# Kernel optimization log

Hardware: AMD Instinct MI355X
Metric: run time of the kernel (lower is better)

The kernel has to match this reference:

```python
import jax, jax.numpy as jnp
import numpy as np

B, S, Y = 2, 4, 4          # samples, n_views (B*S = BS), voxel height vox_xyz_size[1]
BS = B * S

def _bilinear(feat, coords):
    # feat: [C,H,W]; coords: [N,2] normalized (x,y); OOB handled by the valid mask
    C, H, W = feat.shape
    gx, gy = coords[:, 0], coords[:, 1]
    ix = (gx + 1.0) * 0.5 * (W - 1)
    iy = (gy + 1.0) * 0.5 * (H - 1)
    x0 = jnp.floor(ix); y0 = jnp.floor(iy)
    wx = ix - x0; wy = iy - y0
    x0i = jnp.clip(x0.astype(jnp.int32), 0, W - 1); x1i = jnp.clip(x0i + 1, 0, W - 1)
    y0i = jnp.clip(y0.astype(jnp.int32), 0, H - 1); y1i = jnp.clip(y0i + 1, 0, H - 1)
    v00 = feat[:, y0i, x0i]; v01 = feat[:, y0i, x1i]
    v10 = feat[:, y1i, x0i]; v11 = feat[:, y1i, x1i]
    out = (v00 * (1 - wx) * (1 - wy) + v01 * wx * (1 - wy)
           + v10 * (1 - wx) * wy + v11 * wx * wy)            # [C,N]
    valid = (gx >= -1) & (gx <= 1) & (gy >= -1) & (gy <= 1)   # [N]
    return out, valid

def _scale(feat, coords, Zs, Xs, w, b):
    # feat: [BS,C,H,W]; coords: [BS, Y*Zs*Xs, 2]; w: [Co, C*Y]; b: [Co]
    C = feat.shape[1]
    samp, valid = jax.vmap(_bilinear)(feat, coords)           # [BS,C,N], [BS,N]
    samp = samp.reshape(BS, C, Y, Zs * Xs)
    masked = samp * valid.reshape(BS, 1, Y, Zs * Xs).astype(samp.dtype)
    v = masked.reshape(B, S, C * Y, Zs * Xs).max(axis=1)      # max-pool across views
    v = v.reshape(B, C * Y, Zs, Xs)                           # BEV grid
    bev = jax.nn.silu(jnp.einsum('bizx,oi->bozx', v, w) + b[None, :, None, None])
    return bev, valid

def setup_inputs():
    key = jax.random.key(0)
    ks = jax.random.split(key, 9)
    f = jnp.float32
    x3 = jax.random.normal(ks[0], (BS, 256, 64, 64), f)
    x4 = jax.random.normal(ks[1], (BS, 512, 32, 32), f)
    x5 = jax.random.normal(ks[2], (BS, 1024, 16, 16), f)
    coords_s2 = jax.random.uniform(ks[3], (BS, Y * 64 * 64, 2), f) * 2.4 - 1.2
    coords_s4 = jax.random.uniform(ks[4], (BS, Y * 32 * 32, 2), f) * 2.4 - 1.2
    coords_s8 = jax.random.uniform(ks[5], (BS, Y * 16 * 16, 2), f) * 2.4 - 1.2
    w2 = jax.random.normal(ks[6], (256, 256 * Y), f) * 0.02
    b2 = jnp.zeros((256,), f)
    w4 = jax.random.normal(ks[7], (512, 512 * Y), f) * 0.02
    b4 = jnp.zeros((512,), f)
    w8 = jax.random.normal(ks[8], (1024, 1024 * Y), f) * 0.02
    b8 = jnp.zeros((1024,), f)
    return {"x3": x3, "x4": x4, "x5": x5,
            "coords_s2": coords_s2, "coords_s4": coords_s4, "coords_s8": coords_s8,
            "w2": w2, "b2": b2, "w4": w4, "b4": b4, "w8": w8, "b8": b8}

def reference(x3, x4, x5, coords_s2, coords_s4, coords_s8, w2, b2, w4, b4, w8, b8):
    bev2, valid2 = _scale(x3, coords_s2, 64, 64, w2, b2)
    bev4, _ = _scale(x4, coords_s4, 32, 32, w4, b4)
    bev8, _ = _scale(x5, coords_s8, 16, 16, w8, b8)
    valid_vox_mask = valid2.reshape(B, S, -1).max(axis=1).astype(jnp.float32)
    return bev2, bev4, bev8, valid_vox_mask
```

## Files before the change

### kernel.cpp

```cpp
#include <hip/hip_runtime.h>
#include <hip/hip_bf16.h>
#include <math.h>

namespace {

constexpr int B_ = 2;
constexpr int S_ = 4;

typedef short short8 __attribute__((ext_vector_type(8)));
typedef float floatx4 __attribute__((ext_vector_type(4)));
typedef unsigned short ushort4v __attribute__((ext_vector_type(4)));
typedef unsigned short ushort8v __attribute__((ext_vector_type(8)));

__device__ __forceinline__ unsigned short f2bf(float x) {
    union { float f; unsigned u; } a; a.f = x;
    unsigned r = a.u + 0x7fff + ((a.u >> 16) & 1);
    return (unsigned short)(r >> 16);
}
__device__ __forceinline__ float bf2f(unsigned short h) {
    union { unsigned u; float f; } a; a.u = ((unsigned)h) << 16;
    return a.f;
}

__device__ __forceinline__ void transp_tile(
    const float* __restrict__ in, unsigned short* __restrict__ out,
    int C, int P, int bs, int pBase, int cBase, int tid, float (*tile)[33])
{
    int tx = tid & 31;
    int ty = tid >> 5;
    const float* ip = in + ((size_t)bs * C + cBase) * P + pBase;
    #pragma unroll
    for (int r = 0; r < 32; r += 8)
        tile[ty + r][tx] = ip[(size_t)(ty + r) * P + tx];
    __syncthreads();
    unsigned short* op = out + ((size_t)bs * P + pBase) * C + cBase;
    #pragma unroll
    for (int r = 0; r < 32; r += 8)
        op[(size_t)(ty + r) * C + tx] = f2bf(tile[tx][ty + r]);
}

__global__ __launch_bounds__(256) void transpose_all(
    const float* __restrict__ x3, const float* __restrict__ x4, const float* __restrict__ x5,
    unsigned short* __restrict__ f2, unsigned short* __restrict__ f4, unsigned short* __restrict__ f8)
{
    __shared__ float tile[32][33];
    int bid = blockIdx.x;
    int tid = threadIdx.x;
    if (bid < 8192) {
        int local = bid;
        int bs = local >> 10, r = local & 1023;
        transp_tile(x3, f2, 256, 4096, bs, (r & 127) * 32, (r >> 7) * 32, tid, tile);
    } else if (bid < 12288) {
        int local = bid - 8192;
        int bs = local >> 9, r = local & 511;
        transp_tile(x4, f4, 512, 1024, bs, (r & 31) * 32, (r >> 5) * 32, tid, tile);
    } else {
        int local = bid - 12288;
        int bs = local >> 8, r = local & 255;
        transp_tile(x5, f8, 1024, 256, bs, (r & 7) * 32, (r >> 3) * 32, tid, tile);
    }
}

__global__ __launch_bounds__(256) void cvt_w_all(
    const float* __restrict__ w2, const float* __restrict__ w4, const float* __restrict__ w8,
    unsigned short* __restrict__ o2, unsigned short* __restrict__ o4, unsigned short* __restrict__ o8)
{
    int bid = blockIdx.x;
    const float* in; unsigned short* out; int local;
    if (bid < 256)       { in = w2; out = o2; local = bid; }
    else if (bid < 1280) { in = w4; out = o4; local = bid - 256; }
    else                 { in = w8; out = o8; local = bid - 1280; }
    long idx = ((long)local * 256 + threadIdx.x) * 4;
    float4 v = *reinterpret_cast<const float4*>(in + idx);
    ushort4 u;
    u.x = f2bf(v.x); u.y = f2bf(v.y); u.z = f2bf(v.z); u.w = f2bf(v.w);
    *reinterpret_cast<ushort4*>(out + idx) = u;
}

__device__ __forceinline__ void sample_wave(
    const unsigned short* __restrict__ featT, const float* __restrict__ coords,
    unsigned short* __restrict__ vout,
    int Wd, int M, int C, int logM, int logCc, int wid, int lane)
{
    int chunk = wid & ((1 << logCc) - 1);
    int m = (wid >> logCc) & (M - 1);
    int b = wid >> (logCc + logM);
    int c = chunk * 256 + lane * 4;
    int P = Wd * Wd;

    unsigned short outv[16];
    #pragma unroll
    for (int y = 0; y < 4; ++y) {
        float bst0 = -3.4e38f, bst1 = -3.4e38f, bst2 = -3.4e38f, bst3 = -3.4e38f;
        bool anyinv = false;
        #pragma unroll
        for (int s = 0; s < 4; ++s) {
            int bs = b * S_ + s;
            float2 g = ((const float2*)coords)[((size_t)bs << (logM + 2)) + ((size_t)y << logM) + m];
            bool valid = (g.x >= -1.f) && (g.x <= 1.f) && (g.y >= -1.f) && (g.y <= 1.f);
            if (!valid) { anyinv = true; continue; }
            float ix = (g.x + 1.f) * 0.5f * (float)(Wd - 1);
            float iy = (g.y + 1.f) * 0.5f * (float)(Wd - 1);
            float x0f = floorf(ix), y0f = floorf(iy);
            float wx = ix - x0f, wy = iy - y0f;
            int x0 = min(max((int)x0f, 0), Wd - 1);
            int x1 = min(x0 + 1, Wd - 1);
            int y0 = min(max((int)y0f, 0), Wd - 1);
            int y1 = min(y0 + 1, Wd - 1);
            float w00 = (1.f - wx) * (1.f - wy);
            float w01 = wx * (1.f - wy);
            float w10 = (1.f - wx) * wy;
            float w11 = wx * wy;
            const unsigned short* fp = featT + (size_t)bs * P * C + c;
            ushort4v u00 = *reinterpret_cast<const ushort4v*>(fp + (size_t)(y0 * Wd + x0) * C);
            ushort4v u01 = *reinterpret_cast<const ushort4v*>(fp + (size_t)(y0 * Wd + x1) * C);
            ushort4v u10 = *reinterpret_cast<const ushort4v*>(fp + (size_t)(y1 * Wd + x0) * C);
            ushort4v u11 = *reinterpret_cast<const ushort4v*>(fp + (size_t)(y1 * Wd + x1) * C);
            bst0 = fmaxf(bst0, bf2f(u00[0]) * w00 + bf2f(u01[0]) * w01 + bf2f(u10[0]) * w10 + bf2f(u11[0]) * w11);
            bst1 = fmaxf(bst1, bf2f(u00[1]) * w00 + bf2f(u01[1]) * w01 + bf2f(u10[1]) * w10 + bf2f(u11[1]) * w11);
            bst2 = fmaxf(bst2, bf2f(u00[2]) * w00 + bf2f(u01[2]) * w01 + bf2f(u10[2]) * w10 + bf2f(u11[2]) * w11);
            bst3 = fmaxf(bst3, bf2f(u00[3]) * w00 + bf2f(u01[3]) * w01 + bf2f(u10[3]) * w10 + bf2f(u11[3]) * w11);
        }
        if (anyinv) {
            bst0 = fmaxf(bst0, 0.f); bst1 = fmaxf(bst1, 0.f);
            bst2 = fmaxf(bst2, 0.f); bst3 = fmaxf(bst3, 0.f);
        }
        outv[0 * 4 + y] = f2bf(bst0);
        outv[1 * 4 + y] = f2bf(bst1);
        outv[2 * 4 + y] = f2bf(bst2);
        outv[3 * 4 + y] = f2bf(bst3);
    }
    size_t base = (((size_t)b << logM) + m) * ((size_t)C * 4) + chunk * 1024 + lane * 16;
    ushort8v o0, o1;
    #pragma unroll
    for (int t = 0; t < 8; ++t) { o0[t] = outv[t]; o1[t] = outv[8 + t]; }
    *reinterpret_cast<ushort8v*>(vout + base)     = o0;
    *reinterpret_cast<ushort8v*>(vout + base + 8) = o1;
}

__global__ __launch_bounds__(256) void sample_all(
    const unsigned short* __restrict__ f2, const unsigned short* __restrict__ f4,
    const unsigned short* __restrict__ f8,
    const float* __restrict__ c2, const float* __restrict__ c4, const float* __restrict__ c8,
    unsigned short* __restrict__ v2, unsigned short* __restrict__ v4,
    unsigned short* __restrict__ v8)
{
    int gw = (int)((blockIdx.x * 256 + threadIdx.x) >> 6);
    int lane = threadIdx.x & 63;
    if (gw < 8192)
        sample_wave(f2, c2, v2, 64, 4096, 256, 12, 0, gw, lane);
    else if (gw < 12288)
        sample_wave(f4, c4, v4, 32, 1024, 512, 10, 1, gw - 8192, lane);
    else
        sample_wave(f8, c8, v8, 16, 256, 1024, 8, 2, gw - 12288, lane);
}

#define GLOAD(s, it) do { \
    w##s##a = *reinterpret_cast<const float4*>(Wp + (size_t)row0 * K + (it) * 64 + kc); \
    w##s##b = *reinterpret_cast<const float4*>(Wp + (size_t)(row0 + 32) * K + (it) * 64 + kc); \
    v##s##a = *reinterpret_cast<const float4*>(Vp + (size_t)row0 * K + (it) * 64 + kc); \
    v##s##b = *reinterpret_cast<const float4*>(Vp + (size_t)(row0 + 32) * K + (it) * 64 + kc); \
} while (0)

#define LSTORE(s, buf) do { \
    *reinterpret_cast<float4*>(&As[buf][row0 * 72 + kc]) = w##s##a; \
    *reinterpret_cast<float4*>(&As[buf][(row0 + 32) * 72 + kc]) = w##s##b; \
    *reinterpret_cast<float4*>(&Bs[buf][row0 * 72 + kc]) = v##s##a; \
    *reinterpret_cast<float4*>(&Bs[buf][(row0 + 32) * 72 + kc]) = v##s##b; \
} while (0)

#define MFMA_STEP(buf) do { \
    _Pragma("unroll") \
    for (int kss = 0; kss < 64; kss += 32) { \
        short8 af0 = *reinterpret_cast<const short8*>(&As[buf][(wo + lr) * 72 + kss + quad * 8]); \
        short8 af1 = *reinterpret_cast<const short8*>(&As[buf][(wo + 16 + lr) * 72 + kss + quad * 8]); \
        short8 bf0 = *reinterpret_cast<const short8*>(&Bs[buf][(wm + lr) * 72 + kss + quad * 8]); \
        short8 bf1 = *reinterpret_cast<const short8*>(&Bs[buf][(wm + 16 + lr) * 72 + kss + quad * 8]); \
        acc[0][0] = __builtin_amdgcn_mfma_f32_16x16x32_bf16(af0, bf0, acc[0][0], 0, 0, 0); \
        acc[0][1] = __builtin_amdgcn_mfma_f32_16x16x32_bf16(af0, bf1, acc[0][1], 0, 0, 0); \
        acc[1][0] = __builtin_amdgcn_mfma_f32_16x16x32_bf16(af1, bf0, acc[1][0], 0, 0, 0); \
        acc[1][1] = __builtin_amdgcn_mfma_f32_16x16x32_bf16(af1, bf1, acc[1][1], 0, 0, 0); \
    } \
} while (0)

__device__ __forceinline__ void gemm_tile(
    const unsigned short* __restrict__ Wb, const unsigned short* __restrict__ Vb,
    const float* __restrict__ bias, float* __restrict__ out, float* __restrict__ partial,
    int N, int K, int M, int kSplit, int local, int logMt, int logNt,
    int tid, unsigned short (*As)[64 * 72], unsigned short (*Bs)[64 * 72])
{
    const int mTile = local & ((1 << logMt) - 1);
    const int rest  = local >> logMt;
    const int oTile = rest & ((1 << logNt) - 1);
    const int z     = rest >> logNt;
    const int b = z & 1;
    const int ks = z >> 1;
    const int Kspan = K / kSplit;
    const int nIter = Kspan >> 6;

    const int mBase = mTile * 64;
    const int oBase = oTile * 64;
    const int lane = tid & 63;
    const int wave = tid >> 6;
    const int wo = (wave >> 1) * 32;
    const int wm = (wave & 1) * 32;
    const int quad = lane >> 4;
    const int lr = lane & 15;
    const int row0 = tid >> 3;
    const int kc = (tid & 7) * 8;

    const unsigned short* Wp = Wb + (size_t)oBase * K + ks * Kspan;
    const unsigned short* Vp = Vb + ((size_t)b * M + mBase) * K + ks * Kspan;

    floatx4 acc[2][2] = {};
    float4 w0a, w0b, v0a, v0b;
    float4 w1a, w1b, v1a, v1b;

    GLOAD(0, 0);
    LSTORE(0, 0);
    GLOAD(1, 1);
    __syncthreads();

    for (int it = 0; it < nIter; it += 2) {
        MFMA_STEP(0);
        LSTORE(1, 1);
        if (it + 2 < nIter) GLOAD(0, it + 2);
        __syncthreads();
        MFMA_STEP(1);
        if (it + 2 < nIter) {
            LSTORE(0, 0);
            if (it + 3 < nIter) GLOAD(1, it + 3);
            __syncthreads();
        }
    }

    if (kSplit == 1) {
        #pragma unroll
        for (int i = 0; i < 2; ++i)
            #pragma unroll
            for (int r = 0; r < 4; ++r) {
                int o = oBase + wo + i * 16 + quad * 4 + r;
                float bi = bias[o];
                #pragma unroll
                for (int j = 0; j < 2; ++j) {
                    int m = mBase + wm + j * 16 + lr;
                    float x = acc[i][j][r] + bi;
                    out[((size_t)b * N + o) * M + m] = x / (1.f + __expf(-x));
                }
            }
    } else {
        float* pp = partial + (size_t)z * N * M;
        #pragma unroll
        for (int i = 0; i < 2; ++i)
            #pragma unroll
            for (int r = 0; r < 4; ++r) {
                int o = oBase + wo + i * 16 + quad * 4 + r;
                #pragma unroll
                for (int j = 0; j < 2; ++j) {
                    int m = mBase + wm + j * 16 + lr;
                    pp[(size_t)o * M + m] = acc[i][j][r];
                }
            }
    }
}

__global__ __launch_bounds__(256) void gemm_all(
    const unsigned short* __restrict__ w2b, const unsigned short* __restrict__ w4b,
    const unsigned short* __restrict__ w8b,
    const unsigned short* __restrict__ v2, const unsigned short* __restrict__ v4,
    const unsigned short* __restrict__ v8,
    const float* __restrict__ b2, float* __restrict__ bev2,
    float* __restrict__ part4, float* __restrict__ part8)
{
    __shared__ __align__(16) unsigned short As[2][64 * 72];
    __shared__ __align__(16) unsigned short Bs[2][64 * 72];
    int bid = blockIdx.x;
    int tid = threadIdx.x;
    if (bid < 512)
        gemm_tile(w2b, v2, b2, bev2, nullptr, 256, 1024, 4096, 1, bid, 6, 2, tid, As, Bs);
    else if (bid < 1536)
        gemm_tile(w4b, v4, nullptr, nullptr, part4, 512, 2048, 1024, 4, bid - 512, 4, 3, tid, As, Bs);
    else
        gemm_tile(w8b, v8, nullptr, nullptr, part8, 1024, 4096, 256, 8, bid - 1536, 2, 4, tid, As, Bs);
}

__device__ __forceinline__ void reduce_seg(
    const float* __restrict__ partial, const float* __restrict__ bias,
    float* __restrict__ out, int N, int M, int kSplit, size_t idx)
{
    int m4 = M >> 2;
    int mi = (int)(idx % m4);
    int o  = (int)((idx / m4) % N);
    int b  = (int)(idx / ((size_t)m4 * N));
    size_t base = ((size_t)b * N + o) * M + (size_t)mi * 4;
    size_t stride = (size_t)2 * N * M;
    float4 s = *reinterpret_cast<const float4*>(partial + base);
    for (int k = 1; k < kSplit; ++k) {
        float4 t = *reinterpret_cast<const float4*>(partial + base + (size_t)k * stride);
        s.x += t.x; s.y += t.y; s.z += t.z; s.w += t.w;
    }
    float bi = bias[o];
    float xs[4] = {s.x + bi, s.y + bi, s.z + bi, s.w + bi};
    float4 r;
    r.x = xs[0] / (1.f + __expf(-xs[0]));
    r.y = xs[1] / (1.f + __expf(-xs[1]));
    r.z = xs[2] / (1.f + __expf(-xs[2]));
    r.w = xs[3] / (1.f + __expf(-xs[3]));
    *reinterpret_cast<float4*>(out + base) = r;
}

__global__ __launch_bounds__(256) void reduce_mask_all(
    const float* __restrict__ part4, const float* __restrict__ b4, float* __restrict__ bev4,
    const float* __restrict__ part8, const float* __restrict__ b8, float* __restrict__ bev8,
    const float* __restrict__ c2, float* __restrict__ mask)
{
    int bid = blockIdx.x;
    int tid = threadIdx.x;
    if (bid < 1024) {
        reduce_seg(part4, b4, bev4, 512, 1024, 4, (size_t)bid * 256 + tid);
    } else if (bid < 1536) {
        reduce_seg(part8, b8, bev8, 1024, 256, 8, (size_t)(bid - 1024) * 256 + tid);
    } else {
        int idx = (bid - 1536) * 256 + tid;
        int n = idx & 16383;
        int b = idx >> 14;
        float best = 0.f;
        #pragma unroll
        for (int s = 0; s < S_; ++s) {
            float2 g = ((const float2*)c2)[(size_t)(b * S_ + s) * 16384 + n];
            bool valid = (g.x >= -1.f) && (g.x <= 1.f) && (g.y >= -1.f) && (g.y <= 1.f);
            if (valid) best = 1.f;
        }
        mask[idx] = best;
    }
}

}

extern "C" void kernel_launch(void* const* d_in, const int* in_sizes, int n_in,
                              void* d_out, int out_size, void* d_ws, size_t ws_size,
                              hipStream_t stream)
{
    const float* x3 = (const float*)d_in[0];
    const float* x4 = (const float*)d_in[1];
    const float* x5 = (const float*)d_in[2];
    const float* c2 = (const float*)d_in[3];
    const float* c4 = (const float*)d_in[4];
    const float* c8 = (const float*)d_in[5];
    const float* w2 = (const float*)d_in[6];
    const float* b2 = (const float*)d_in[7];
    const float* w4 = (const float*)d_in[8];
    const float* b4 = (const float*)d_in[9];
    const float* w8 = (const float*)d_in[10];
    const float* b8 = (const float*)d_in[11];

    float* out  = (float*)d_out;
    float* bev2 = out;
    float* bev4 = bev2 + (long)2 * 256 * 64 * 64;
    float* bev8 = bev4 + (long)2 * 512 * 32 * 32;
    float* mask = bev8 + (long)2 * 1024 * 16 * 16;

    char* ws = (char*)d_ws;
    unsigned short* f2v  = (unsigned short*)(ws);
    unsigned short* f4v  = (unsigned short*)(ws + (16L << 20));
    unsigned short* f8v  = (unsigned short*)(ws + (24L << 20));
    unsigned short* v2v  = (unsigned short*)(ws + (28L << 20));
    unsigned short* v4v  = (unsigned short*)(ws + (44L << 20));
    unsigned short* v8v  = (unsigned short*)(ws + (52L << 20));
    unsigned short* w2bf = (unsigned short*)(ws + (56L << 20));
    unsigned short* w4bf = (unsigned short*)(ws + (57L << 20));
    unsigned short* w8bf = (unsigned short*)(ws + (59L << 20));
    float*          part4 = (float*)(ws + (68L << 20));
    float*          part8 = (float*)(ws + (84L << 20));

    transpose_all<<<dim3(14336), 256, 0, stream>>>(x3, x4, x5, f2v, f4v, f8v);
    cvt_w_all<<<dim3(5376), 256, 0, stream>>>(w2, w4, w8, w2bf, w4bf, w8bf);
    sample_all<<<dim3(3584), 256, 0, stream>>>(f2v, f4v, f8v, c2, c4, c8, v2v, v4v, v8v);
    gemm_all<<<dim3(2560), 256, 0, stream>>>(w2bf, w4bf, w8bf, v2v, v4v, v8v,
                                             b2, bev2, part4, part8);
    reduce_mask_all<<<dim3(1664), 256, 0, stream>>>(part4, b4, bev4, part8, b8, bev8,
                                                    c2, mask);
}
```

Baseline: 210.0 us.

## Precompute bilinear coordinate table, merge prep kernels, and widen sampling to 8 channels

Transposes, weight conversion, a new coordinate-prep pass and the validity mask are merged into one launch. The prep pass stores packed bilinear corner indices and fp16 weights per sample. The sampling kernel reads this table instead of recomputing coordinates for every channel chunk, and each lane loads 8 bf16 channels per corner instead of 4, halving the wave count. This removes one kernel launch and redundant coordinate math, at the cost of an extra table in the workspace and fp16-rounded interpolation weights.

```diff
diff --git a/kernel.cpp b/kernel.cpp
--- a/kernel.cpp
+++ b/kernel.cpp
@@ -4,12 +4,8 @@
 
 namespace {
 
-constexpr int B_ = 2;
-constexpr int S_ = 4;
-
 typedef short short8 __attribute__((ext_vector_type(8)));
 typedef float floatx4 __attribute__((ext_vector_type(4)));
-typedef unsigned short ushort4v __attribute__((ext_vector_type(4)));
 typedef unsigned short ushort8v __attribute__((ext_vector_type(8)));
 
 __device__ __forceinline__ unsigned short f2bf(float x) {
@@ -20,6 +16,16 @@
 __device__ __forceinline__ float bf2f(unsigned short h) {
     union { unsigned u; float f; } a; a.u = ((unsigned)h) << 16;
     return a.f;
+}
+__device__ __forceinline__ unsigned f2h(float x) {
+    _Float16 h = (_Float16)x;
+    unsigned short u; __builtin_memcpy(&u, &h, 2);
+    return u;
+}
+__device__ __forceinline__ float h2f(unsigned u) {
+    unsigned short us = (unsigned short)u;
+    _Float16 h; __builtin_memcpy(&h, &us, 2);
+    return (float)h;
 }
 
 __device__ __forceinline__ void transp_tile(
@@ -39,120 +45,162 @@
         op[(size_t)(ty + r) * C + tx] = f2bf(tile[tx][ty + r]);
 }
 
-__global__ __launch_bounds__(256) void transpose_all(
+__device__ __forceinline__ void coord_prep(
+    const float* __restrict__ coords, uint4* __restrict__ table, int Wd, int idx)
+{
+    float2 g = ((const float2*)coords)[idx];
+    uint4 e;
+    bool valid = (g.x >= -1.f) && (g.x <= 1.f) && (g.y >= -1.f) && (g.y <= 1.f);
+    if (!valid) {
+        e.x = 0xFFFFFFFFu; e.y = 0u; e.z = 0u; e.w = 0u;
+    } else {
+        float ix = (g.x + 1.f) * 0.5f * (float)(Wd - 1);
+        float iy = (g.y + 1.f) * 0.5f * (float)(Wd - 1);
+        float x0f = floorf(ix), y0f = floorf(iy);
+        float wx = ix - x0f, wy = iy - y0f;
+        int x0 = min(max((int)x0f, 0), Wd - 1);
+        int x1 = min(x0 + 1, Wd - 1);
+        int y0 = min(max((int)y0f, 0), Wd - 1);
+        int y1 = min(y0 + 1, Wd - 1);
+        unsigned p00 = y0 * Wd + x0, p01 = y0 * Wd + x1;
+        unsigned p10 = y1 * Wd + x0, p11 = y1 * Wd + x1;
+        e.x = p00 | (p01 << 16);
+        e.y = p10 | (p11 << 16);
+        e.z = f2h((1.f - wx) * (1.f - wy)) | (f2h(wx * (1.f - wy)) << 16);
+        e.w = f2h((1.f - wx) * wy)         | (f2h(wx * wy) << 16);
+    }
+    table[idx] = e;
+}
+
+__global__ __launch_bounds__(256) void prep_all(
     const float* __restrict__ x3, const float* __restrict__ x4, const float* __restrict__ x5,
-    unsigned short* __restrict__ f2, unsigned short* __restrict__ f4, unsigned short* __restrict__ f8)
+    unsigned short* __restrict__ f2, unsigned short* __restrict__ f4, unsigned short* __restrict__ f8,
+    const float* __restrict__ w2, const float* __restrict__ w4, const float* __restrict__ w8,
+    unsigned short* __restrict__ o2, unsigned short* __restrict__ o4, unsigned short* __restrict__ o8,
+    const float* __restrict__ c2, const float* __restrict__ c4, const float* __restrict__ c8,
+    uint4* __restrict__ t2, uint4* __restrict__ t4, uint4* __restrict__ t8,
+    float* __restrict__ mask)
 {
     __shared__ float tile[32][33];
     int bid = blockIdx.x;
     int tid = threadIdx.x;
     if (bid < 8192) {
-        int local = bid;
-        int bs = local >> 10, r = local & 1023;
+        int bs = bid >> 10, r = bid & 1023;
         transp_tile(x3, f2, 256, 4096, bs, (r & 127) * 32, (r >> 7) * 32, tid, tile);
     } else if (bid < 12288) {
         int local = bid - 8192;
         int bs = local >> 9, r = local & 511;
         transp_tile(x4, f4, 512, 1024, bs, (r & 31) * 32, (r >> 5) * 32, tid, tile);
-    } else {
+    } else if (bid < 14336) {
         int local = bid - 12288;
         int bs = local >> 8, r = local & 255;
         transp_tile(x5, f8, 1024, 256, bs, (r & 7) * 32, (r >> 3) * 32, tid, tile);
-    }
-}
-
-__global__ __launch_bounds__(256) void cvt_w_all(
-    const float* __restrict__ w2, const float* __restrict__ w4, const float* __restrict__ w8,
-    unsigned short* __restrict__ o2, unsigned short* __restrict__ o4, unsigned short* __restrict__ o8)
-{
-    int bid = blockIdx.x;
-    const float* in; unsigned short* out; int local;
-    if (bid < 256)       { in = w2; out = o2; local = bid; }
-    else if (bid < 1280) { in = w4; out = o4; local = bid - 256; }
-    else                 { in = w8; out = o8; local = bid - 1280; }
-    long idx = ((long)local * 256 + threadIdx.x) * 4;
-    float4 v = *reinterpret_cast<const float4*>(in + idx);
-    ushort4 u;
-    u.x = f2bf(v.x); u.y = f2bf(v.y); u.z = f2bf(v.z); u.w = f2bf(v.w);
-    *reinterpret_cast<ushort4*>(out + idx) = u;
-}
-
-__device__ __forceinline__ void sample_wave(
-    const unsigned short* __restrict__ featT, const float* __restrict__ coords,
+    } else if (bid < 19712) {
+        int local = bid - 14336;
+        const float* in; unsigned short* out;
+        if (local < 256)       { in = w2; out = o2; }
+        else if (local < 1280) { in = w4; out = o4; local -= 256; }
+        else                   { in = w8; out = o8; local -= 1280; }
+        long idx = ((long)local * 256 + tid) * 4;
+        float4 v = *reinterpret_cast<const float4*>(in + idx);
+        ushort4 u;
+        u.x = f2bf(v.x); u.y = f2bf(v.y); u.z = f2bf(v.z); u.w = f2bf(v.w);
+        *reinterpret_cast<ushort4*>(out + idx) = u;
+    } else if (bid < 20224) {
+        coord_prep(c2, t2, 64, (bid - 19712) * 256 + tid);
+    } else if (bid < 20352) {
+        coord_prep(c4, t4, 32, (bid - 20224) * 256 + tid);
+    } else if (bid < 20384) {
+        coord_prep(c8, t8, 16, (bid - 20352) * 256 + tid);
+    } else {
+        int idx = (bid - 20384) * 256 + tid;
+        int n = idx & 16383;
+        int b = idx >> 14;
+        float best = 0.f;
+        #pragma unroll
+        for (int s = 0; s < 4; ++s) {
+            float2 g = ((const float2*)c2)[(size_t)(b * 4 + s) * 16384 + n];
+            bool valid = (g.x >= -1.f) && (g.x <= 1.f) && (g.y >= -1.f) && (g.y <= 1.f);
+            if (valid) best = 1.f;
+        }
+        mask[idx] = best;
+    }
+}
+
+__device__ __forceinline__ void sample_wave_v4(
+    const unsigned short* __restrict__ featT, const uint4* __restrict__ table,
     unsigned short* __restrict__ vout,
-    int Wd, int M, int C, int logM, int logCc, int wid, int lane)
-{
-    int chunk = wid & ((1 << logCc) - 1);
-    int m = (wid >> logCc) & (M - 1);
-    int b = wid >> (logCc + logM);
-    int c = chunk * 256 + lane * 4;
-    int P = Wd * Wd;
-
-    unsigned short outv[16];
+    int P, int M, int C, int logM, int mwLog, int ckLog, int wid, int lane)
+{
+    int cover = 64 >> mwLog;
+    int dm = (mwLog ? (lane >> (6 - mwLog)) : 0);
+    int laneInM = lane & (cover - 1);
+    int chunk = wid & ((1 << ckLog) - 1);
+    int rest = wid >> ckLog;
+    int mg = rest & ((M >> mwLog) - 1);
+    int b = rest >> (logM - mwLog);
+    int m = (mg << mwLog) + dm;
+    int ch = chunk * (cover * 8) + laneInM * 8;
+
+    unsigned short outv[32];
     #pragma unroll
     for (int y = 0; y < 4; ++y) {
-        float bst0 = -3.4e38f, bst1 = -3.4e38f, bst2 = -3.4e38f, bst3 = -3.4e38f;
+        float bst[8];
+        #pragma unroll
+        for (int j = 0; j < 8; ++j) bst[j] = -3.4e38f;
         bool anyinv = false;
         #pragma unroll
         for (int s = 0; s < 4; ++s) {
-            int bs = b * S_ + s;
-            float2 g = ((const float2*)coords)[((size_t)bs << (logM + 2)) + ((size_t)y << logM) + m];
-            bool valid = (g.x >= -1.f) && (g.x <= 1.f) && (g.y >= -1.f) && (g.y <= 1.f);
-            if (!valid) { anyinv = true; continue; }
-            float ix = (g.x + 1.f) * 0.5f * (float)(Wd - 1);
-            float iy = (g.y + 1.f) * 0.5f * (float)(Wd - 1);
-            float x0f = floorf(ix), y0f = floorf(iy);
-            float wx = ix - x0f, wy = iy - y0f;
-            int x0 = min(max((int)x0f, 0), Wd - 1);
-            int x1 = min(x0 + 1, Wd - 1);
-            int y0 = min(max((int)y0f, 0), Wd - 1);
-            int y1 = min(y0 + 1, Wd - 1);
-            float w00 = (1.f - wx) * (1.f - wy);
-            float w01 = wx * (1.f - wy);
-            float w10 = (1.f - wx) * wy;
-            float w11 = wx * wy;
-            const unsigned short* fp = featT + (size_t)bs * P * C + c;
-            ushort4v u00 = *reinterpret_cast<const ushort4v*>(fp + (size_t)(y0 * Wd + x0) * C);
-            ushort4v u01 = *reinterpret_cast<const ushort4v*>(fp + (size_t)(y0 * Wd + x1) * C);
-            ushort4v u10 = *reinterpret_cast<const ushort4v*>(fp + (size_t)(y1 * Wd + x0) * C);
-            ushort4v u11 = *reinterpret_cast<const ushort4v*>(fp + (size_t)(y1 * Wd + x1) * C);
-            bst0 = fmaxf(bst0, bf2f(u00[0]) * w00 + bf2f(u01[0]) * w01 + bf2f(u10[0]) * w10 + bf2f(u11[0]) * w11);
-            bst1 = fmaxf(bst1, bf2f(u00[1]) * w00 + bf2f(u01[1]) * w01 + bf2f(u10[1]) * w10 + bf2f(u11[1]) * w11);
-            bst2 = fmaxf(bst2, bf2f(u00[2]) * w00 + bf2f(u01[2]) * w01 + bf2f(u10[2]) * w10 + bf2f(u11[2]) * w11);
-            bst3 = fmaxf(bst3, bf2f(u00[3]) * w00 + bf2f(u01[3]) * w01 + bf2f(u10[3]) * w10 + bf2f(u11[3]) * w11);
+            int bs = b * 4 + s;
+            uint4 e = table[(((size_t)bs * 4 + y) << logM) + m];
+            if ((e.x & 0xffffu) == 0xffffu) { anyinv = true; continue; }
+            unsigned p00 = e.x & 0xffffu, p01 = e.x >> 16;
+            unsigned p10 = e.y & 0xffffu, p11 = e.y >> 16;
+            float w00 = h2f(e.z & 0xffffu), w01 = h2f(e.z >> 16);
+            float w10 = h2f(e.w & 0xffffu), w11 = h2f(e.w >> 16);
+            const unsigned short* fp = featT + (size_t)bs * P * C + ch;
+            ushort8v u00 = *reinterpret_cast<const ushort8v*>(fp + (size_t)p00 * C);
+            ushort8v u01 = *reinterpret_cast<const ushort8v*>(fp + (size_t)p01 * C);
+            ushort8v u10 = *reinterpret_cast<const ushort8v*>(fp + (size_t)p10 * C);
+            ushort8v u11 = *reinterpret_cast<const ushort8v*>(fp + (size_t)p11 * C);
+            #pragma unroll
+            for (int j = 0; j < 8; ++j) {
+                float v = bf2f(u00[j]) * w00 + bf2f(u01[j]) * w01
+                        + bf2f(u10[j]) * w10 + bf2f(u11[j]) * w11;
+                bst[j] = fmaxf(bst[j], v);
+            }
         }
-        if (anyinv) {
-            bst0 = fmaxf(bst0, 0.f); bst1 = fmaxf(bst1, 0.f);
-            bst2 = fmaxf(bst2, 0.f); bst3 = fmaxf(bst3, 0.f);
+        #pragma unroll
+        for (int j = 0; j < 8; ++j) {
+            float v = anyinv ? fmaxf(bst[j], 0.f) : bst[j];
+            outv[j * 4 + y] = f2bf(v);
         }
-        outv[0 * 4 + y] = f2bf(bst0);
-        outv[1 * 4 + y] = f2bf(bst1);
-        outv[2 * 4 + y] = f2bf(bst2);
-        outv[3 * 4 + y] = f2bf(bst3);
-    }
-    size_t base = (((size_t)b << logM) + m) * ((size_t)C * 4) + chunk * 1024 + lane * 16;
-    ushort8v o0, o1;
+    }
+    size_t base = (((size_t)b << logM) + m) * ((size_t)C * 4) + (size_t)ch * 4;
     #pragma unroll
-    for (int t = 0; t < 8; ++t) { o0[t] = outv[t]; o1[t] = outv[8 + t]; }
-    *reinterpret_cast<ushort8v*>(vout + base)     = o0;
-    *reinterpret_cast<ushort8v*>(vout + base + 8) = o1;
+    for (int t = 0; t < 4; ++t) {
+        ushort8v o;
+        #pragma unroll
+        for (int q = 0; q < 8; ++q) o[q] = outv[t * 8 + q];
+        *reinterpret_cast<ushort8v*>(vout + base + t * 8) = o;
+    }
 }
 
 __global__ __launch_bounds__(256) void sample_all(
     const unsigned short* __restrict__ f2, const unsigned short* __restrict__ f4,
     const unsigned short* __restrict__ f8,
-    const float* __restrict__ c2, const float* __restrict__ c4, const float* __restrict__ c8,
+    const uint4* __restrict__ t2, const uint4* __restrict__ t4, const uint4* __restrict__ t8,
     unsigned short* __restrict__ v2, unsigned short* __restrict__ v4,
     unsigned short* __restrict__ v8)
 {
     int gw = (int)((blockIdx.x * 256 + threadIdx.x) >> 6);
     int lane = threadIdx.x & 63;
-    if (gw < 8192)
-        sample_wave(f2, c2, v2, 64, 4096, 256, 12, 0, gw, lane);
-    else if (gw < 12288)
-        sample_wave(f4, c4, v4, 32, 1024, 512, 10, 1, gw - 8192, lane);
+    if (gw < 4096)
+        sample_wave_v4(f2, t2, v2, 4096, 4096, 256, 12, 1, 0, gw, lane);
+    else if (gw < 6144)
+        sample_wave_v4(f4, t4, v4, 1024, 1024, 512, 10, 0, 0, gw - 4096, lane);
     else
-        sample_wave(f8, c8, v8, 16, 256, 1024, 8, 2, gw - 12288, lane);
+        sample_wave_v4(f8, t8, v8, 256, 256, 1024, 8, 0, 1, gw - 6144, lane);
 }
 
 #define GLOAD(s, it) do { \
@@ -309,30 +357,16 @@
     *reinterpret_cast<float4*>(out + base) = r;
 }
 
-__global__ __launch_bounds__(256) void reduce_mask_all(
+__global__ __launch_bounds__(256) void reduce_all(
     const float* __restrict__ part4, const float* __restrict__ b4, float* __restrict__ bev4,
-    const float* __restrict__ part8, const float* __restrict__ b8, float* __restrict__ bev8,
-    const float* __restrict__ c2, float* __restrict__ mask)
+    const float* __restrict__ part8, const float* __restrict__ b8, float* __restrict__ bev8)
 {
     int bid = blockIdx.x;
     int tid = threadIdx.x;
-    if (bid < 1024) {
+    if (bid < 1024)
         reduce_seg(part4, b4, bev4, 512, 1024, 4, (size_t)bid * 256 + tid);
-    } else if (bid < 1536) {
+    else
         reduce_seg(part8, b8, bev8, 1024, 256, 8, (size_t)(bid - 1024) * 256 + tid);
-    } else {
-        int idx = (bid - 1536) * 256 + tid;
-        int n = idx & 16383;
-        int b = idx >> 14;
-        float best = 0.f;
-        #pragma unroll
-        for (int s = 0; s < S_; ++s) {
-            float2 g = ((const float2*)c2)[(size_t)(b * S_ + s) * 16384 + n];
-            bool valid = (g.x >= -1.f) && (g.x <= 1.f) && (g.y >= -1.f) && (g.y <= 1.f);
-            if (valid) best = 1.f;
-        }
-        mask[idx] = best;
-    }
 }
 
 }
@@ -372,12 +406,18 @@
     unsigned short* w8bf = (unsigned short*)(ws + (59L << 20));
     float*          part4 = (float*)(ws + (68L << 20));
     float*          part8 = (float*)(ws + (84L << 20));
-
-    transpose_all<<<dim3(14336), 256, 0, stream>>>(x3, x4, x5, f2v, f4v, f8v);
-    cvt_w_all<<<dim3(5376), 256, 0, stream>>>(w2, w4, w8, w2bf, w4bf, w8bf);
-    sample_all<<<dim3(3584), 256, 0, stream>>>(f2v, f4v, f8v, c2, c4, c8, v2v, v4v, v8v);
-    gemm_all<<<dim3(2560), 256, 0, stream>>>(w2bf, w4bf, w8bf, v2v, v4v, v8v,
-                                             b2, bev2, part4, part8);
-    reduce_mask_all<<<dim3(1664), 256, 0, stream>>>(part4, b4, bev4, part8, b8, bev8,
-                                                    c2, mask);
-}
+    uint4*          t2v   = (uint4*)(ws + (100L << 20));
+    uint4*          t4v   = (uint4*)(ws + (102L << 20));
+    uint4*          t8v   = (uint4*)(ws + (102L << 20) + (1L << 19));
+
+    prep_all<<<dim3(20512), 256, 0, stream>>>(
+        x3, x4, x5, f2v, f4v, f8v,
+        w2, w4, w8, w2bf, w4bf, w8bf,
+        c2, c4, c8, t2v, t4v, t8v, mask);
+    sample_all<<<dim3(1792), 256, 0, stream>>>(
+        f2v, f4v, f8v, t2v, t4v, t8v, v2v, v4v, v8v);
+    gemm_all<<<dim3(2560), 256, 0, stream>>>(
+        w2bf, w4bf, w8bf, v2v, v4v, v8v, b2, bev2, part4, part8);
+    reduce_all<<<dim3(1536), 256, 0, stream>>>(
+        part4, b4, bev4, part8, b8, bev8);
+}
```

After: 219.4 us. 4.5% more time.
